# Optimization experiments

Hardware: AMD Instinct MI355X
Metric: run time of the kernel (lower is better)

Reference implementation:

```python
import jax, jax.numpy as jnp
import numpy as np

BN_EPS = 1e-5


def setup_inputs() -> dict:
    key = jax.random.key(0)
    ks = jax.random.split(key, 12)
    N, K, C_IN, C_OUT = 50000, 16, 128, 128
    C2 = 2 * C_OUT
    return {
        "features": jax.random.normal(ks[0], (N, C_IN), dtype=jnp.float32),
        "neighbor_idx": jax.random.randint(ks[1], (N, K), 0, N, dtype=jnp.int64),
        "W1": jax.random.normal(ks[2], (C_IN, C2), dtype=jnp.float32) * 0.05,
        "b1": jax.random.normal(ks[3], (C2,), dtype=jnp.float32) * 0.05,
        "gamma": jax.random.uniform(ks[4], (C2,), dtype=jnp.float32, minval=0.5, maxval=1.5),
        "beta": jax.random.normal(ks[5], (C2,), dtype=jnp.float32) * 0.05,
        "run_mean": jax.random.normal(ks[6], (C2,), dtype=jnp.float32) * 0.05,
        "run_var": jax.random.uniform(ks[7], (C2,), dtype=jnp.float32, minval=0.5, maxval=1.5),
        "Ws": jax.random.normal(ks[8], (C2, C2), dtype=jnp.float32) * 0.05,
        "Wm": jax.random.normal(ks[9], (C2, C_OUT), dtype=jnp.float32) * 0.05,
        "bm": jax.random.normal(ks[10], (C_OUT,), dtype=jnp.float32) * 0.05,
    }


def reference(features, neighbor_idx, W1, b1, gamma, beta, run_mean, run_var, Ws, Wm, bm):
    # mlp1: Linear + ReLU (no BN)
    x = jax.nn.relu(features @ W1 + b1)                     # (N, 2C)
    # gather_neighbour: irregular index_select
    g = x[neighbor_idx]                                     # (N, k, 2C)
    # BatchNorm1d over channel dim (inference semantics, running stats)
    inv = gamma * jax.lax.rsqrt(run_var + BN_EPS)
    g = (g - run_mean) * inv + beta                         # (N, k, 2C)
    # AttentivePooling: per-neighbor score linear (no bias), softmax over k
    scores = jax.nn.softmax(g @ Ws, axis=1)                 # (N, k, 2C)
    feat = jnp.sum(scores * g, axis=1)                      # (N, 2C)
    return feat @ Wm + bm                                   # (N, C_out)
```

## Files before the change

### kernel.cpp

```cpp
#include <hip/hip_runtime.h>
#include <cstddef>

#define C_IN  128
#define C2    256
#define C_OUT 128
#define KNBR  16
#define PTS   32

typedef unsigned short u16;
typedef __attribute__((ext_vector_type(8))) short bf16x8;
typedef __attribute__((ext_vector_type(8))) unsigned short u16x8;
typedef __attribute__((ext_vector_type(4))) float f32x4;

__device__ __forceinline__ float bf2f(u16 h) {
    return __uint_as_float(((unsigned int)h) << 16);
}
__device__ __forceinline__ u16 f2bf(float x) {
    unsigned int u = __float_as_uint(x);
    return (u16)((u + 0x7fffu + ((u >> 16) & 1u)) >> 16);
}

__global__ void prep_k(const float* __restrict__ W1, const float* __restrict__ Ws,
                       const float* __restrict__ Wm, const float* __restrict__ b1,
                       const float* __restrict__ gamma, const float* __restrict__ beta,
                       const float* __restrict__ mean, const float* __restrict__ var,
                       u16* __restrict__ W1t, u16* __restrict__ Wst,
                       u16* __restrict__ Wmt, float4* __restrict__ bnp)
{
    const int n = blockIdx.x, t = threadIdx.x;
    if (blockIdx.y == 0) {
        if (t < 128) W1t[n * 128 + t] = f2bf(W1[t * 256 + n]);
    } else if (blockIdx.y == 1) {
        Wst[n * 256 + t] = f2bf(Ws[t * 256 + n]);
    } else if (blockIdx.y == 2) {
        if (n < 128) Wmt[n * 256 + t] = f2bf(Wm[t * 128 + n]);
    } else if (n == 0) {
        float iv = gamma[t] * rsqrtf(var[t] + 1e-5f);
        bnp[t] = make_float4(b1[t], iv, beta[t] - mean[t] * iv, 0.f);
    }
}


__global__ __launch_bounds__(256)
void mlp_k(const float* __restrict__ F, const u16* __restrict__ W1t,
           const u16* __restrict__ Wst, const float4* __restrict__ bnp,
           u16* __restrict__ packed, int N)
{
    __shared__ u16 As[64][136];
    __shared__ u16 Bs[128][72];
    __shared__ u16 xs[64][264];

    const int tid = threadIdx.x;
    const int w = tid >> 6, l = tid & 63, q = l >> 4, r = l & 15;
    const int wm = w & 1, wn = w >> 1;
    const int m0 = blockIdx.x * 64;

    #pragma unroll
    for (int i = 0; i < 8; i++) {
        int idx = tid + i * 256;
        int row = idx >> 5, c4 = (idx & 31) * 4;
        int gm = m0 + row;
        float4 v = make_float4(0.f, 0.f, 0.f, 0.f);
        if (gm < N) v = *(const float4*)(F + (size_t)gm * C_IN + c4);
        ushort4 h;
        h.x = f2bf(v.x); h.y = f2bf(v.y); h.z = f2bf(v.z); h.w = f2bf(v.w);
        *(ushort4*)&As[row][c4] = h;
    }

    ushort4 xr[2][2][4];

    #pragma unroll
    for (int nh = 0; nh < 2; nh++) {
        f32x4 acc[2][4] = {};
        #pragma unroll 1
        for (int k0 = 0; k0 < C_IN; k0 += 64) {
            __syncthreads();
            #pragma unroll
            for (int i = 0; i < 4; i++) {
                int idx = tid + i * 256;
                int row = idx >> 3, g = (idx & 7) * 8;
                *(uint4*)&Bs[row][g] = *(const uint4*)(
                    W1t + (size_t)(nh * 128 + row) * C_IN + k0 + g);
            }
            __syncthreads();
            #pragma unroll
            for (int h = 0; h < 2; h++) {
                bf16x8 af[2], bfr[4];
                #pragma unroll
                for (int i = 0; i < 2; i++)
                    af[i] = *(const bf16x8*)&As[wm * 32 + i * 16 + r][k0 + h * 32 + q * 8];
                #pragma unroll
                for (int j = 0; j < 4; j++)
                    bfr[j] = *(const bf16x8*)&Bs[wn * 64 + j * 16 + r][h * 32 + q * 8];
                #pragma unroll
                for (int i = 0; i < 2; i++)
                    #pragma unroll
                    for (int j = 0; j < 4; j++)
                        acc[i][j] = __builtin_amdgcn_mfma_f32_16x16x32_bf16(
                            af[i], bfr[j], acc[i][j], 0, 0, 0);
            }
        }
        #pragma unroll
        for (int j = 0; j < 4; j++) {
            const int ch = nh * 128 + wn * 64 + j * 16 + r;
            const float4 bp = bnp[ch];
            #pragma unroll
            for (int i = 0; i < 2; i++) {
                const int mb = wm * 32 + i * 16 + q * 4;
                ushort4 hx;
                #pragma unroll
                for (int p = 0; p < 4; p++) {
                    float x = fmaxf(acc[i][j][p] + bp.x, 0.f) * bp.y + bp.z;
                    u16 h = f2bf(x);
                    xs[mb + p][ch] = h;
                    if (p == 0) hx.x = h; else if (p == 1) hx.y = h;
                    else if (p == 2) hx.z = h; else hx.w = h;
                }
                xr[nh][i][j] = hx;
            }
        }
    }

    #pragma unroll
    for (int nh = 0; nh < 2; nh++) {
        f32x4 acc[2][4] = {};
        #pragma unroll 1
        for (int k0 = 0; k0 < C2; k0 += 64) {
            __syncthreads();
            #pragma unroll
            for (int i = 0; i < 4; i++) {
                int idx = tid + i * 256;
                int row = idx >> 3, g = (idx & 7) * 8;
                *(uint4*)&Bs[row][g] = *(const uint4*)(
                    Wst + (size_t)(nh * 128 + row) * C2 + k0 + g);
            }
            __syncthreads();
            #pragma unroll
            for (int h = 0; h < 2; h++) {
                bf16x8 af[2], bfr[4];
                #pragma unroll
                for (int i = 0; i < 2; i++)
                    af[i] = *(const bf16x8*)&xs[wm * 32 + i * 16 + r][k0 + h * 32 + q * 8];
                #pragma unroll
                for (int j = 0; j < 4; j++)
                    bfr[j] = *(const bf16x8*)&Bs[wn * 64 + j * 16 + r][h * 32 + q * 8];
                #pragma unroll
                for (int i = 0; i < 2; i++)
                    #pragma unroll
                    for (int j = 0; j < 4; j++)
                        acc[i][j] = __builtin_amdgcn_mfma_f32_16x16x32_bf16(
                            af[i], bfr[j], acc[i][j], 0, 0, 0);
            }
        }
        #pragma unroll
        for (int j = 0; j < 4; j++) {
            const int ch = nh * 128 + wn * 64 + j * 16 + r;
            #pragma unroll
            for (int i = 0; i < 2; i++) {
                const int mb = wm * 32 + i * 16 + q * 4;
                const ushort4 hx = xr[nh][i][j];
                #pragma unroll
                for (int p = 0; p < 4; p++) {
                    const int gm = m0 + mb + p;
                    if (gm < N) {
                        unsigned xv = (p == 0) ? hx.x : (p == 1) ? hx.y
                                    : (p == 2) ? hx.z : hx.w;
                        unsigned ey = f2bf(__expf(acc[i][j][p]));
                        *(unsigned*)(packed + (size_t)gm * 512 + ch * 2) =
                            ey | (xv << 16);
                    }
                }
            }
        }
    }
}

__global__ __launch_bounds__(256, 5)
void gather_out_k(const u16* __restrict__ packed, const int* __restrict__ nidx,
                  const u16* __restrict__ Bt, const float* __restrict__ bias,
                  float* __restrict__ Cf, int N)
{
    __shared__ int rows[PTS * KNBR];
    __shared__ __align__(16) u16 fsm[PTS * 264];

    const int tid = threadIdx.x;
    const int w = tid >> 6, l = tid & 63, q = l >> 4, r = l & 15;
    const int m0 = blockIdx.x * PTS;

    #pragma unroll
    for (int i = 0; i < 2; i++) {
        int idx = tid + i * 256;
        int n = m0 + (idx >> 4);
        rows[idx] = (n < N) ? nidx[n * KNBR + (idx & 15)] : 0;
    }
    __syncthreads();

    #pragma unroll 1
    for (int ip = 0; ip < 8; ip++) {
        const int pl = w * 8 + ip;
        float num[4] = {0.f, 0.f, 0.f, 0.f};
        float den[4] = {0.f, 0.f, 0.f, 0.f};
        #pragma unroll 1
        for (int hf = 0; hf < 2; hf++) {
            u16x8 v[8];
            #pragma unroll
            for (int k = 0; k < 8; k++)
                v[k] = *(const u16x8*)(packed +
                    (size_t)rows[pl * KNBR + hf * 8 + k] * 512 + l * 8);
            #pragma unroll
            for (int k = 0; k < 8; k++) {
                #pragma unroll
                for (int c = 0; c < 4; c++) {
                    float e = bf2f((u16)v[k][2 * c]);
                    float x = bf2f((u16)v[k][2 * c + 1]);
                    den[c] += e;
                    num[c] = fmaf(e, x, num[c]);
                }
            }
        }
        ushort4 o;
        o.x = f2bf(num[0] / den[0]); o.y = f2bf(num[1] / den[1]);
        o.z = f2bf(num[2] / den[2]); o.w = f2bf(num[3] / den[3]);
        *(ushort4*)&fsm[pl * 264 + l * 4] = o;
    }
    __syncthreads();

    const int wm = w & 1, wn = w >> 1;
    f32x4 acc[4] = {};

    #pragma unroll
    for (int k0 = 0; k0 < C2; k0 += 64) {
        #pragma unroll
        for (int h = 0; h < 2; h++) {
            bf16x8 af, bfr[4];
            af = *(const bf16x8*)&fsm[(wm * 16 + r) * 264 + k0 + h * 32 + q * 8];
            #pragma unroll
            for (int j = 0; j < 4; j++)
                bfr[j] = *(const bf16x8*)(Bt +
                    (size_t)(wn * 64 + j * 16 + r) * C2 + k0 + h * 32 + q * 8);
            #pragma unroll
            for (int j = 0; j < 4; j++)
                acc[j] = __builtin_amdgcn_mfma_f32_16x16x32_bf16(
                    af, bfr[j], acc[j], 0, 0, 0);
        }
    }
    __syncthreads();

    float* STF = (float*)fsm;
    #pragma unroll
    for (int j = 0; j < 4; j++) {
        const int ch = wn * 64 + j * 16 + r;
        const float bo = bias[ch];
        const int mb = wm * 16 + q * 4;
        #pragma unroll
        for (int p = 0; p < 4; p++)
            STF[(mb + p) * 132 + ch] = acc[j][p] + bo;
    }
    __syncthreads();
    #pragma unroll
    for (int i = 0; i < 4; i++) {
        int idx = tid + i * 256;
        int row = idx >> 5, c4 = (idx & 31) * 4;
        if (m0 + row < N)
            *(float4*)(Cf + (size_t)(m0 + row) * C_OUT + c4) =
                *(const float4*)&STF[row * 132 + c4];
    }
}

extern "C" void kernel_launch(void* const* d_in, const int* in_sizes, int n_in,
                              void* d_out, int out_size, void* d_ws, size_t ws_size,
                              hipStream_t stream)
{
    const float* features = (const float*)d_in[0];
    const int*   nidx     = (const int*)d_in[1];
    const float* W1       = (const float*)d_in[2];
    const float* b1       = (const float*)d_in[3];
    const float* gamma    = (const float*)d_in[4];
    const float* beta     = (const float*)d_in[5];
    const float* mean     = (const float*)d_in[6];
    const float* var      = (const float*)d_in[7];
    const float* Ws       = (const float*)d_in[8];
    const float* Wm       = (const float*)d_in[9];
    const float* bm       = (const float*)d_in[10];
    float* out = (float*)d_out;

    const int N = in_sizes[0] / C_IN;

    u16* packed = (u16*)d_ws;
    u16* W1t    = packed + (size_t)N * 512;
    u16* Wst    = W1t + 256 * 128;
    u16* Wmt    = Wst + 256 * 256;
    float4* bnp = (float4*)(Wmt + 128 * 256);

    prep_k<<<dim3(256, 4), 256, 0, stream>>>(W1, Ws, Wm, b1, gamma, beta,
                                             mean, var, W1t, Wst, Wmt, bnp);

    const int MT = (N + 63) / 64;
    const int GT = (N + PTS - 1) / PTS;

    mlp_k<<<MT, 256, 0, stream>>>(features, W1t, Wst, bnp, packed, N);
    gather_out_k<<<GT, 256, 0, stream>>>(packed, nidx, Wmt, bm, out, N);
}
```

Measured before the change: 244.0 us.

## Load mlp A operand straight into registers and split gather launch in two

mlp_k now loads each wave's A fragments directly from global memory into bf16 registers instead of staging them through a shared-memory tile. That cuts LDS usage and the shared-memory round trip, and the launch bound now asks for 3 blocks per CU. The gather kernel takes a block offset and is launched twice, with 521 blocks first and the rest second. The split likely targets tail or wave-quantization effects, at the cost of an extra launch. The register-held A fragments raise register pressure.

```diff
diff --git a/kernel.cpp b/kernel.cpp
--- a/kernel.cpp
+++ b/kernel.cpp
@@ -41,12 +41,11 @@
 }
 
 
-__global__ __launch_bounds__(256)
+__global__ __launch_bounds__(256, 3)
 void mlp_k(const float* __restrict__ F, const u16* __restrict__ W1t,
            const u16* __restrict__ Wst, const float4* __restrict__ bnp,
            u16* __restrict__ packed, int N)
 {
-    __shared__ u16 As[64][136];
     __shared__ u16 Bs[128][72];
     __shared__ u16 xs[64][264];
 
@@ -55,16 +54,25 @@
     const int wm = w & 1, wn = w >> 1;
     const int m0 = blockIdx.x * 64;
 
-    #pragma unroll
-    for (int i = 0; i < 8; i++) {
-        int idx = tid + i * 256;
-        int row = idx >> 5, c4 = (idx & 31) * 4;
-        int gm = m0 + row;
-        float4 v = make_float4(0.f, 0.f, 0.f, 0.f);
-        if (gm < N) v = *(const float4*)(F + (size_t)gm * C_IN + c4);
-        ushort4 h;
-        h.x = f2bf(v.x); h.y = f2bf(v.y); h.z = f2bf(v.z); h.w = f2bf(v.w);
-        *(ushort4*)&As[row][c4] = h;
+    bf16x8 af1[2][4];
+    #pragma unroll
+    for (int i = 0; i < 2; i++) {
+        const int gr = m0 + wm * 32 + i * 16 + r;
+        #pragma unroll
+        for (int t = 0; t < 4; t++) {
+            float4 v0 = make_float4(0.f, 0.f, 0.f, 0.f), v1 = v0;
+            if (gr < N) {
+                const float* s = F + (size_t)gr * C_IN + t * 32 + q * 8;
+                v0 = *(const float4*)s;
+                v1 = *(const float4*)(s + 4);
+            }
+            bf16x8 a;
+            a[0] = (short)f2bf(v0.x); a[1] = (short)f2bf(v0.y);
+            a[2] = (short)f2bf(v0.z); a[3] = (short)f2bf(v0.w);
+            a[4] = (short)f2bf(v1.x); a[5] = (short)f2bf(v1.y);
+            a[6] = (short)f2bf(v1.z); a[7] = (short)f2bf(v1.w);
+            af1[i][t] = a;
+        }
     }
 
     ushort4 xr[2][2][4];
@@ -85,10 +93,8 @@
             __syncthreads();
             #pragma unroll
             for (int h = 0; h < 2; h++) {
-                bf16x8 af[2], bfr[4];
-                #pragma unroll
-                for (int i = 0; i < 2; i++)
-                    af[i] = *(const bf16x8*)&As[wm * 32 + i * 16 + r][k0 + h * 32 + q * 8];
+                const int kt = (k0 >> 5) + h;
+                bf16x8 bfr[4];
                 #pragma unroll
                 for (int j = 0; j < 4; j++)
                     bfr[j] = *(const bf16x8*)&Bs[wn * 64 + j * 16 + r][h * 32 + q * 8];
@@ -97,7 +103,7 @@
                     #pragma unroll
                     for (int j = 0; j < 4; j++)
                         acc[i][j] = __builtin_amdgcn_mfma_f32_16x16x32_bf16(
-                            af[i], bfr[j], acc[i][j], 0, 0, 0);
+                            af1[i][kt], bfr[j], acc[i][j], 0, 0, 0);
             }
         }
         #pragma unroll
@@ -178,14 +184,14 @@
 __global__ __launch_bounds__(256, 5)
 void gather_out_k(const u16* __restrict__ packed, const int* __restrict__ nidx,
                   const u16* __restrict__ Bt, const float* __restrict__ bias,
-                  float* __restrict__ Cf, int N)
+                  float* __restrict__ Cf, int b0, int N)
 {
     __shared__ int rows[PTS * KNBR];
     __shared__ __align__(16) u16 fsm[PTS * 264];
 
     const int tid = threadIdx.x;
     const int w = tid >> 6, l = tid & 63, q = l >> 4, r = l & 15;
-    const int m0 = blockIdx.x * PTS;
+    const int m0 = (b0 + blockIdx.x) * PTS;
 
     #pragma unroll
     for (int i = 0; i < 2; i++) {
@@ -297,7 +303,9 @@
 
     const int MT = (N + 63) / 64;
     const int GT = (N + PTS - 1) / PTS;
+    const int G1 = 521;
 
     mlp_k<<<MT, 256, 0, stream>>>(features, W1t, Wst, bnp, packed, N);
-    gather_out_k<<<GT, 256, 0, stream>>>(packed, nidx, Wmt, bm, out, N);
-}
+    gather_out_k<<<G1, 256, 0, stream>>>(packed, nidx, Wmt, bm, out, 0, N);
+    gather_out_k<<<GT - G1, 256, 0, stream>>>(packed, nidx, Wmt, bm, out, G1, N);
+}
```

Measured after the change: 279.4 us. 1.15x slower.
